# Kernel optimization log

Hardware: AMD Instinct MI355X
Metric: run time of the kernel (lower is better)

## Reference

```python
import jax, jax.numpy as jnp
import numpy as np

DIM = 1024
HEADS = 16
HEAD_DIM = DIM // HEADS
SCALE = HEAD_DIM ** -0.5


def apply_rope(x, theta=10000.0):
    # x: [b, h, n, d]
    n, d = x.shape[2], x.shape[3]
    seq = jnp.arange(n, dtype=jnp.float32)
    inv = 1.0 / (theta ** (jnp.arange(0, d, 2, dtype=jnp.float32) / d))  # [d/2]
    freqs = seq[:, None] * inv[None, :]  # [n, d/2]
    cos = jnp.cos(freqs)[None, None]  # [1,1,n,d/2]
    sin = jnp.sin(freqs)[None, None]
    x1, x2 = jnp.split(x, 2, axis=-1)
    return jnp.concatenate([x1 * cos - x2 * sin, x1 * sin + x2 * cos], axis=-1)


def setup_inputs() -> dict:
    key = jax.random.key(0)
    ks = jax.random.split(key, 7)
    s = DIM ** -0.5
    return {
        "x": jax.random.normal(ks[0], (2, 2048, DIM), dtype=jnp.float32),
        "Wqkv": jax.random.normal(ks[1], (3 * DIM, DIM), dtype=jnp.float32) * s,
        "bqkv": jax.random.normal(ks[2], (3 * DIM,), dtype=jnp.float32) * 0.02,
        "Wpre": jax.random.normal(ks[3], (HEADS, HEADS), dtype=jnp.float32) * HEADS ** -0.5,
        "Wpost": jax.random.normal(ks[4], (HEADS, HEADS), dtype=jnp.float32) * HEADS ** -0.5,
        "Wout": jax.random.normal(ks[5], (DIM, DIM), dtype=jnp.float32) * s,
        "bout": jax.random.normal(ks[6], (DIM,), dtype=jnp.float32) * 0.02,
    }


def reference(x, Wqkv, bqkv, Wpre, Wpost, Wout, bout):
    b, n, _ = x.shape
    qkv = x @ Wqkv.T + bqkv  # [b, n, 3*dim]
    q, k, v = jnp.split(qkv, 3, axis=-1)
    # [b, n, dim] -> [b, h, n, d]
    reshape = lambda t: t.reshape(b, n, HEADS, HEAD_DIM).transpose(0, 2, 1, 3)
    q, k, v = reshape(q), reshape(k), reshape(v)
    q = apply_rope(q)
    k = apply_rope(k)
    logits = jnp.einsum('bhid,bhjd->bhij', q, k) * SCALE
    # pre-softmax talking heads: Linear(heads->heads), y[...,g] = sum_h x[...,h] * Wpre[g,h]
    logits = jnp.einsum('bhij,gh->bgij', logits, Wpre)
    attn = jax.nn.softmax(logits, axis=-1)
    attn = jnp.einsum('bhij,gh->bgij', attn, Wpost)
    out = jnp.einsum('bhij,bhjd->bhid', attn, v)
    out = out.transpose(0, 2, 1, 3).reshape(b, n, DIM)
    return out @ Wout.T + bout
```

## Files before the change

### kernel.cpp

```cpp
#include <hip/hip_runtime.h>
#include <cstddef>
#include <cstdint>

#define SEQ    2048
#define DMODEL 1024
#define NHEAD  16
#define HDIM   64
#define SCALE  0.125f
#define LOG2E  1.4426950408889634f

typedef _Float16 f16;
typedef unsigned short u16;
typedef unsigned int   u32;
typedef __attribute__((ext_vector_type(8))) _Float16 h8v;
typedef __attribute__((ext_vector_type(4))) _Float16 h4v;
typedef __attribute__((ext_vector_type(4))) float    f4v;

__device__ __forceinline__ u32 pkh(float a, float b) {
    u16 x = __builtin_bit_cast(u16, (f16)a);
    u16 y = __builtin_bit_cast(u16, (f16)b);
    return (u32)x | ((u32)y << 16);
}

__device__ __forceinline__ float fexp2(float x) {
#if __has_builtin(__builtin_amdgcn_exp2f)
    return __builtin_amdgcn_exp2f(x);
#else
    return exp2f(x);
#endif
}

__device__ __forceinline__ f4v mfma32(h8v a, h8v b, f4v c) {
    return __builtin_amdgcn_mfma_f32_16x16x32_f16(a, b, c, 0, 0, 0);
}
__device__ __forceinline__ f4v mfma16(h4v a, h4v b, f4v c) {
    return __builtin_amdgcn_mfma_f32_16x16x16f16(a, b, c, 0, 0, 0);
}

__global__ __launch_bounds__(256)
void cvt_f16_kernel(const float* __restrict__ x, const float* __restrict__ Wqkv,
                    const float* __restrict__ Wout,
                    f16* __restrict__ Xh, f16* __restrict__ Wqh, f16* __restrict__ Woh)
{
    size_t i = ((size_t)blockIdx.x * 256 + threadIdx.x) * 8;
    const float* src; f16* dst; size_t off;
    if (i < 4194304)      { src = x;    dst = Xh;  off = i; }
    else if (i < 7340032) { src = Wqkv; dst = Wqh; off = i - 4194304; }
    else                  { src = Wout; dst = Woh; off = i - 7340032; }
    float4 a = *(const float4*)&src[off];
    float4 b = *(const float4*)&src[off + 4];
    uint4 o;
    o.x = pkh(a.x, a.y); o.y = pkh(a.z, a.w);
    o.z = pkh(b.x, b.y); o.w = pkh(b.z, b.w);
    *(uint4*)&dst[off] = o;
}

__global__ __launch_bounds__(256)
void gemm_f16_kernel(const f16* __restrict__ A, const f16* __restrict__ B,
                     const float* __restrict__ bias, void* __restrict__ Cout,
                     int N, int K, int mode)
{
    __shared__ __align__(16) char Asb[8192];
    __shared__ __align__(16) char Bsb[8192];
    int tid = threadIdx.x;
    int w = tid >> 6, l = tid & 63, lr = l & 15, lc = l >> 4;
    int row0 = blockIdx.y * 128, col0 = blockIdx.x * 128;
    int wr = (w >> 1) * 64, wc = (w & 1) * 64;

    f4v acc[4][4];
    #pragma unroll
    for (int m = 0; m < 4; ++m)
        #pragma unroll
        for (int n = 0; n < 4; ++n) acc[m][n] = (f4v){0.f, 0.f, 0.f, 0.f};

    int r0 = tid >> 2, k0s = tid & 3;
    int r1 = (tid + 256) >> 2, k1s = tid & 3;

    uint4 ra0, ra1, rb0, rb1;
    ra0 = *(const uint4*)&A[(size_t)(row0 + r0) * K + k0s * 8];
    ra1 = *(const uint4*)&A[(size_t)(row0 + r1) * K + k1s * 8];
    rb0 = *(const uint4*)&B[(size_t)(col0 + r0) * K + k0s * 8];
    rb1 = *(const uint4*)&B[(size_t)(col0 + r1) * K + k1s * 8];

    int NT = K >> 5;
    for (int kt = 0; kt < NT; ++kt) {
        *(uint4*)(Asb + r0 * 64 + ((k0s ^ (r0 & 3)) << 4)) = ra0;
        *(uint4*)(Asb + r1 * 64 + ((k1s ^ (r1 & 3)) << 4)) = ra1;
        *(uint4*)(Bsb + r0 * 64 + ((k0s ^ (r0 & 3)) << 4)) = rb0;
        *(uint4*)(Bsb + r1 * 64 + ((k1s ^ (r1 & 3)) << 4)) = rb1;
        if (kt + 1 < NT) {
            int kk = (kt + 1) * 32;
            ra0 = *(const uint4*)&A[(size_t)(row0 + r0) * K + kk + k0s * 8];
            ra1 = *(const uint4*)&A[(size_t)(row0 + r1) * K + kk + k1s * 8];
            rb0 = *(const uint4*)&B[(size_t)(col0 + r0) * K + kk + k0s * 8];
            rb1 = *(const uint4*)&B[(size_t)(col0 + r1) * K + kk + k1s * 8];
        }
        __syncthreads();
        h8v af[4], bf[4];
        #pragma unroll
        for (int m = 0; m < 4; ++m) {
            int row = wr + m * 16 + lr;
            af[m] = *(h8v*)(Asb + row * 64 + ((lc ^ (row & 3)) << 4));
        }
        #pragma unroll
        for (int n = 0; n < 4; ++n) {
            int col = wc + n * 16 + lr;
            bf[n] = *(h8v*)(Bsb + col * 64 + ((lc ^ (col & 3)) << 4));
        }
        #pragma unroll
        for (int m = 0; m < 4; ++m)
            #pragma unroll
            for (int n = 0; n < 4; ++n)
                acc[m][n] = mfma32(af[m], bf[n], acc[m][n]);
        __syncthreads();
    }

    #pragma unroll
    for (int m = 0; m < 4; ++m)
        #pragma unroll
        for (int r = 0; r < 4; ++r) {
            int row = row0 + wr + m * 16 + lc * 4 + r;
            #pragma unroll
            for (int n = 0; n < 4; ++n) {
                int col = col0 + wc + n * 16 + lr;
                float v = acc[m][n][r] + bias[col];
                if (mode == 0) ((f16*)Cout)[(size_t)row * N + col] = (f16)v;
                else           ((float*)Cout)[(size_t)row * N + col] = v;
            }
        }
}

__global__ __launch_bounds__(256)
void pack_qk_kernel(const f16* __restrict__ QKVh, f16* __restrict__ Qh, f16* __restrict__ Kh)
{
    int gid = blockIdx.x * 256 + threadIdx.x;
    int i     = gid & 15;
    int t8    = (gid >> 4) & 3;
    int h     = (gid >> 6) & 15;
    int rh    = (gid >> 10) & 255;
    int which = (gid >> 18) & 1;
    int row = rh * 16 + i;
    int pos = row & (SEQ - 1);
    int b   = row >> 11;
    f16* dst = which ? Kh : Qh;

    h8v x1 = *(const h8v*)&QKVh[(size_t)row * 3072 + which * 1024 + h * 64 + t8 * 8];
    h8v x2 = *(const h8v*)&QKVh[(size_t)row * 3072 + which * 1024 + h * 64 + t8 * 8 + 32];

    float y1[8], y2[8];
    #pragma unroll
    for (int e = 0; e < 8; ++e) {
        int t = t8 * 8 + e;
        float inv = exp2f((float)(-2 * t) * (0.015625f * 13.287712379549449f));
        float ang = (float)pos * inv;
        float c, s;
        sincosf(ang, &s, &c);
        float a1 = (float)x1[e], a2 = (float)x2[e];
        y1[e] = a1 * c - a2 * s;
        y2[e] = a1 * s + a2 * c;
    }
    int it = pos >> 4;
    size_t b0 = (((((size_t)(b*128 + it)*16 + h)*2 + 0)*4 + t8)*16 + i)*8;
    size_t b1 = (((((size_t)(b*128 + it)*16 + h)*2 + 1)*4 + t8)*16 + i)*8;
    uint4 o0, o1;
    o0.x = pkh(y1[0], y1[1]); o0.y = pkh(y1[2], y1[3]);
    o0.z = pkh(y1[4], y1[5]); o0.w = pkh(y1[6], y1[7]);
    o1.x = pkh(y2[0], y2[1]); o1.y = pkh(y2[2], y2[3]);
    o1.z = pkh(y2[4], y2[5]); o1.w = pkh(y2[6], y2[7]);
    *(uint4*)(dst + b0) = o0;
    *(uint4*)(dst + b1) = o1;
}

__global__ __launch_bounds__(256)
void pack_v_kernel(const f16* __restrict__ QKVh, f16* __restrict__ Vt)
{
    int gid = blockIdx.x * 256 + threadIdx.x;
    int dd = gid & 15;
    int jc = (gid >> 4) & 3;
    int dt = (gid >> 6) & 3;
    int g  = (gid >> 8) & 15;
    int jt = (gid >> 12) & 63;
    int b  = (gid >> 18) & 1;
    int d = g * 64 + dt * 16 + dd;
    f16 v[8];
    #pragma unroll
    for (int e = 0; e < 8; ++e) {
        int j = jt * 32 + jc * 8 + e;
        v[e] = QKVh[(size_t)(b * SEQ + j) * 3072 + 2048 + d];
    }
    size_t off = ((((((size_t)b*64 + jt)*16 + g)*4 + dt)*4 + jc)*16 + dd)*8;
    uint4 o;
    o.x = pkh((float)v[0], (float)v[1]); o.y = pkh((float)v[2], (float)v[3]);
    o.z = pkh((float)v[4], (float)v[5]); o.w = pkh((float)v[6], (float)v[7]);
    *(uint4*)(Vt + off) = o;
}

__global__ __launch_bounds__(256)
void pack_ctx_kernel(const f16* __restrict__ Cp, f16* __restrict__ Ch)
{
    size_t i = ((size_t)blockIdx.x * 256 + threadIdx.x) * 8;
    h8v p0 = *(const h8v*)&Cp[i];
    h8v p1 = *(const h8v*)&Cp[i + 4194304];
    h8v p2 = *(const h8v*)&Cp[i + 8388608];
    h8v p3 = *(const h8v*)&Cp[i + 12582912];
    float s[8];
    #pragma unroll
    for (int e = 0; e < 8; ++e)
        s[e] = (float)p0[e] + (float)p1[e] + (float)p2[e] + (float)p3[e];
    uint4 o;
    o.x = pkh(s[0], s[1]); o.y = pkh(s[2], s[3]);
    o.z = pkh(s[4], s[5]); o.w = pkh(s[6], s[7]);
    *(uint4*)&Ch[i] = o;
}

template<int FULL>
__global__ __launch_bounds__(1024, 1)
void attn_core(const f16* __restrict__ Qh, const f16* __restrict__ Kh,
               const f16* __restrict__ Vt, const float* __restrict__ Wpre,
               const float* __restrict__ Wpost, const float* __restrict__ Zp,
               float* __restrict__ Zout, f16* __restrict__ Octx)
{
    __shared__ __align__(16) char ss[32768];
    __shared__ __align__(16) char es[FULL ? 32768 : 16];
    __shared__ float zred[FULL ? 512 : 8192];

    int tid = threadIdx.x;
    int wv = tid >> 6;
    int l  = tid & 63;
    int lr = l & 15;
    int lc = l >> 4;

    int bid   = blockIdx.x;
    int it2   = bid & 63;
    int b     = (bid >> 6) & 1;
    int split = bid >> 7;

    h4v wpre4;
    #pragma unroll
    for (int e = 0; e < 4; ++e) wpre4[e] = (f16)(Wpre[lr * 16 + lc * 4 + e] * (SCALE * LOG2E));
    h4v wpost;
    if (FULL) {
        #pragma unroll
        for (int e = 0; e < 4; ++e) wpost[e] = (f16)Wpost[lr * 16 + lc * 4 + e];
    }

    h8v qf[2][2];
    #pragma unroll
    for (int itl = 0; itl < 2; ++itl)
        #pragma unroll
        for (int ks = 0; ks < 2; ++ks) {
            size_t off = ((((size_t)((b*128 + it2*2 + itl)*16 + wv)*2 + ks)*4 + lc)*16 + lr)*8;
            qf[itl][ks] = *(const h8v*)(Qh + off);
        }

    if (FULL && tid < 512) {
        int itl = tid >> 8, g = (tid >> 4) & 15, i = tid & 15;
        size_t idx = (size_t)(b * 16 + g) * SEQ + it2 * 32 + itl * 16 + i;
        zred[tid] = log2f(Zp[idx] + Zp[65536 + idx] + Zp[131072 + idx] + Zp[196608 + idx]);
    }
    __syncthreads();

    float m4[2][4];
    if (FULL) {
        #pragma unroll
        for (int itl = 0; itl < 2; ++itl)
            #pragma unroll
            for (int r = 0; r < 4; ++r)
                m4[itl][r] = zred[itl * 256 + (lc * 4 + r) * 16 + lr];
    }

    f4v pv[2][4];
    if (FULL) {
        #pragma unroll
        for (int itl = 0; itl < 2; ++itl)
            #pragma unroll
            for (int dt = 0; dt < 4; ++dt) pv[itl][dt] = (f4v){0.f, 0.f, 0.f, 0.f};
    }
    float zacc[2][4] = {};

    int j0beg = split * 512;
    int jtbeg = j0beg >> 4;

    for (int s = 0; s < 16; ++s) {
        h8v kf[2][2];
        #pragma unroll
        for (int js = 0; js < 2; ++js)
            #pragma unroll
            for (int ks = 0; ks < 2; ++ks) {
                size_t off = ((((size_t)((b*128 + jtbeg + s*2 + js)*16 + wv)*2 + ks)*4 + lc)*16 + lr)*8;
                kf[js][ks] = *(const h8v*)(Kh + off);
            }
        h8v vf[4];
        if (FULL) {
            int jt32 = (j0beg >> 5) + s;
            #pragma unroll
            for (int dt = 0; dt < 4; ++dt) {
                size_t voff = (((((size_t)(b*64 + jt32)*16 + wv)*4 + dt)*4 + lc)*16 + lr)*8;
                vf[dt] = *(const h8v*)(Vt + voff);
            }
        }

        #pragma unroll
        for (int itl = 0; itl < 2; ++itl)
            #pragma unroll
            for (int js = 0; js < 2; ++js) {
                f4v q = (f4v){0.f, 0.f, 0.f, 0.f};
                q = mfma32(qf[itl][0], kf[js][0], q);
                q = mfma32(qf[itl][1], kf[js][1], q);
                #pragma unroll
                for (int r = 0; r < 4; ++r) {
                    int i = lc * 4 + r;
                    int addr = itl * 16384 + ((wv >> 2) * 2 + js) * 2048
                             + i * 128 + ((lr ^ i) << 3) + (wv & 3) * 2;
                    *(u16*)(ss + addr) = __builtin_bit_cast(u16, (f16)q[r]);
                }
            }
        __syncthreads();

        #pragma unroll
        for (int itl = 0; itl < 2; ++itl) {
            u32 a2p[4];
            #pragma unroll
            for (int tt = 0; tt < 2; ++tt) {
                int t = wv * 2 + tt;
                int addr = itl * 16384 + (lc * 2 + (t >> 4)) * 2048
                         + lr * 128 + (((t & 15) ^ lr) << 3);
                union { uint2 u; h4v v; } cv;
                cv.u = *(uint2*)(ss + addr);
                f4v s1 = mfma16(wpre4, cv.v, (f4v){0.f, 0.f, 0.f, 0.f});
                if (!FULL) {
                    #pragma unroll
                    for (int r = 0; r < 4; ++r) zacc[itl][r] += fexp2(s1[r]);
                } else {
                    h4v pf;
                    #pragma unroll
                    for (int r = 0; r < 4; ++r) pf[r] = (f16)fexp2(s1[r] - m4[itl][r]);
                    f4v a2 = mfma16(wpost, pf, (f4v){0.f, 0.f, 0.f, 0.f});
                    #pragma unroll
                    for (int r = 0; r < 4; ++r) {
                        u32 v = (u32)__builtin_bit_cast(u16, (f16)a2[r]);
                        if (tt) a2p[r] |= v << 16;
                        else    a2p[r]  = v;
                    }
                }
            }
            if (FULL) {
                #pragma unroll
                for (int r = 0; r < 4; ++r) {
                    int gq = lc * 4 + r;
                    int off = itl * 16384 + ((gq * 1024 + lr * 64 + wv * 4) ^ ((lr & 7) << 4));
                    *(u32*)(es + off) = a2p[r];
                }
            }
        }
        __syncthreads();

        if (FULL) {
            #pragma unroll
            for (int itl = 0; itl < 2; ++itl) {
                h8v af = *(h8v*)(es + itl * 16384
                                 + ((wv * 1024 + lr * 64 + lc * 16) ^ ((lr & 7) << 4)));
                #pragma unroll
                for (int dt = 0; dt < 4; ++dt)
                    pv[itl][dt] = mfma32(af, vf[dt], pv[itl][dt]);
            }
        }
    }

    if (!FULL) {
        #pragma unroll
        for (int itl = 0; itl < 2; ++itl)
            #pragma unroll
            for (int r = 0; r < 4; ++r)
                zred[itl * 4096 + ((lc * 4 + r) * 16 + lr) * 16 + wv] = zacc[itl][r];
        __syncthreads();
        if (tid < 512) {
            int itl = tid >> 8, gi = tid & 255;
            float z = 0.f;
            #pragma unroll
            for (int w2 = 0; w2 < 16; ++w2) z += zred[itl * 4096 + gi * 16 + w2];
            int g = gi >> 4, i = gi & 15;
            Zout[(size_t)split * 65536 + (size_t)(b * 16 + g) * SEQ + it2 * 32 + itl * 16 + i] = z;
        }
    } else {
        f16* dst = Octx + (size_t)split * 4194304;
        #pragma unroll
        for (int itl = 0; itl < 2; ++itl)
            #pragma unroll
            for (int dt = 0; dt < 4; ++dt)
                #pragma unroll
                for (int r = 0; r < 4; ++r) {
                    int row = it2 * 32 + itl * 16 + lc * 4 + r;
                    int col = wv * 64 + dt * 16 + lr;
                    dst[(size_t)(b * SEQ + row) * DMODEL + col] = (f16)pv[itl][dt][r];
                }
    }
}

extern "C" void kernel_launch(void* const* d_in, const int* in_sizes, int n_in,
                              void* d_out, int out_size, void* d_ws, size_t ws_size,
                              hipStream_t stream)
{
    const float* x     = (const float*)d_in[0];
    const float* Wqkv  = (const float*)d_in[1];
    const float* bqkv  = (const float*)d_in[2];
    const float* Wpre  = (const float*)d_in[3];
    const float* Wpost = (const float*)d_in[4];
    const float* Wout  = (const float*)d_in[5];
    const float* bout  = (const float*)d_in[6];
    float* out = (float*)d_out;

    float* ws = (float*)d_ws;
    f16*   QKVh = (f16*)(ws);
    f16*   CTXp = (f16*)(ws);
    f16*   Xh   = (f16*)(ws + 8388608);
    f16*   Wqh  = (f16*)(ws + 10485760);
    f16*   Woh  = (f16*)(ws + 12058624);
    f16*   Qh   = (f16*)(ws + 12582912);
    f16*   Kh   = (f16*)(ws + 14680064);
    f16*   Vt   = (f16*)(ws + 16777216);
    f16*   Ch   = (f16*)(ws + 18874368);
    float* Zp   = ws + 19922944;

    dim3 blk(256);
    cvt_f16_kernel<<<4096, blk, 0, stream>>>(x, Wqkv, Wout, Xh, Wqh, Woh);
    gemm_f16_kernel<<<dim3(24, 32), blk, 0, stream>>>(Xh, Wqh, bqkv, (void*)QKVh, 3072, 1024, 0);
    pack_qk_kernel<<<2048, blk, 0, stream>>>(QKVh, Qh, Kh);
    pack_v_kernel<<<2048, blk, 0, stream>>>(QKVh, Vt);
    attn_core<0><<<512, dim3(1024), 0, stream>>>(Qh, Kh, Vt, Wpre, Wpost, nullptr, Zp, nullptr);
    attn_core<1><<<512, dim3(1024), 0, stream>>>(Qh, Kh, Vt, Wpre, Wpost, Zp, nullptr, CTXp);
    pack_ctx_kernel<<<2048, blk, 0, stream>>>(CTXp, Ch);
    gemm_f16_kernel<<<dim3(8, 32), blk, 0, stream>>>(Ch, Woh, bout, (void*)out, 1024, 1024, 1);
}
```

Before: 220.9 us.

## Fuse f16 conversion and split reduction into GEMM loads; double attention key tile

```diff
diff --git a/kernel.cpp b/kernel.cpp
--- a/kernel.cpp
+++ b/kernel.cpp
@@ -37,28 +37,24 @@
     return __builtin_amdgcn_mfma_f32_16x16x16f16(a, b, c, 0, 0, 0);
 }
 
+__device__ __forceinline__ uint4 cvt8(const float* __restrict__ p) {
+    float4 a = *(const float4*)p;
+    float4 b = *(const float4*)(p + 4);
+    return make_uint4(pkh(a.x, a.y), pkh(a.z, a.w), pkh(b.x, b.y), pkh(b.z, b.w));
+}
+
+__device__ __forceinline__ uint4 sum4(const f16* __restrict__ p) {
+    h8v s = *(const h8v*)p;
+    s = s + *(const h8v*)(p + 4194304);
+    s = s + *(const h8v*)(p + 8388608);
+    s = s + *(const h8v*)(p + 12582912);
+    union { h8v v; uint4 u; } c; c.v = s;
+    return c.u;
+}
+
 __global__ __launch_bounds__(256)
-void cvt_f16_kernel(const float* __restrict__ x, const float* __restrict__ Wqkv,
-                    const float* __restrict__ Wout,
-                    f16* __restrict__ Xh, f16* __restrict__ Wqh, f16* __restrict__ Woh)
-{
-    size_t i = ((size_t)blockIdx.x * 256 + threadIdx.x) * 8;
-    const float* src; f16* dst; size_t off;
-    if (i < 4194304)      { src = x;    dst = Xh;  off = i; }
-    else if (i < 7340032) { src = Wqkv; dst = Wqh; off = i - 4194304; }
-    else                  { src = Wout; dst = Woh; off = i - 7340032; }
-    float4 a = *(const float4*)&src[off];
-    float4 b = *(const float4*)&src[off + 4];
-    uint4 o;
-    o.x = pkh(a.x, a.y); o.y = pkh(a.z, a.w);
-    o.z = pkh(b.x, b.y); o.w = pkh(b.z, b.w);
-    *(uint4*)&dst[off] = o;
-}
-
-__global__ __launch_bounds__(256)
-void gemm_f16_kernel(const f16* __restrict__ A, const f16* __restrict__ B,
-                     const float* __restrict__ bias, void* __restrict__ Cout,
-                     int N, int K, int mode)
+void gemm_qkv_kernel(const float* __restrict__ A, const float* __restrict__ B,
+                     const float* __restrict__ bias, f16* __restrict__ C)
 {
     __shared__ __align__(16) char Asb[8192];
     __shared__ __align__(16) char Bsb[8192];
@@ -73,27 +69,25 @@
         #pragma unroll
         for (int n = 0; n < 4; ++n) acc[m][n] = (f4v){0.f, 0.f, 0.f, 0.f};
 
-    int r0 = tid >> 2, k0s = tid & 3;
-    int r1 = (tid + 256) >> 2, k1s = tid & 3;
-
-    uint4 ra0, ra1, rb0, rb1;
-    ra0 = *(const uint4*)&A[(size_t)(row0 + r0) * K + k0s * 8];
-    ra1 = *(const uint4*)&A[(size_t)(row0 + r1) * K + k1s * 8];
-    rb0 = *(const uint4*)&B[(size_t)(col0 + r0) * K + k0s * 8];
-    rb1 = *(const uint4*)&B[(size_t)(col0 + r1) * K + k1s * 8];
-
-    int NT = K >> 5;
-    for (int kt = 0; kt < NT; ++kt) {
-        *(uint4*)(Asb + r0 * 64 + ((k0s ^ (r0 & 3)) << 4)) = ra0;
-        *(uint4*)(Asb + r1 * 64 + ((k1s ^ (r1 & 3)) << 4)) = ra1;
-        *(uint4*)(Bsb + r0 * 64 + ((k0s ^ (r0 & 3)) << 4)) = rb0;
-        *(uint4*)(Bsb + r1 * 64 + ((k1s ^ (r1 & 3)) << 4)) = rb1;
-        if (kt + 1 < NT) {
+    int r0 = tid >> 2, ks = tid & 3;
+    int r1 = r0 + 64;
+
+    uint4 ra0 = cvt8(&A[(size_t)(row0 + r0) * 1024 + ks * 8]);
+    uint4 ra1 = cvt8(&A[(size_t)(row0 + r1) * 1024 + ks * 8]);
+    uint4 rb0 = cvt8(&B[(size_t)(col0 + r0) * 1024 + ks * 8]);
+    uint4 rb1 = cvt8(&B[(size_t)(col0 + r1) * 1024 + ks * 8]);
+
+    for (int kt = 0; kt < 32; ++kt) {
+        *(uint4*)(Asb + r0 * 64 + ((ks ^ (r0 & 3)) << 4)) = ra0;
+        *(uint4*)(Asb + r1 * 64 + ((ks ^ (r1 & 3)) << 4)) = ra1;
+        *(uint4*)(Bsb + r0 * 64 + ((ks ^ (r0 & 3)) << 4)) = rb0;
+        *(uint4*)(Bsb + r1 * 64 + ((ks ^ (r1 & 3)) << 4)) = rb1;
+        if (kt + 1 < 32) {
             int kk = (kt + 1) * 32;
-            ra0 = *(const uint4*)&A[(size_t)(row0 + r0) * K + kk + k0s * 8];
-            ra1 = *(const uint4*)&A[(size_t)(row0 + r1) * K + kk + k1s * 8];
-            rb0 = *(const uint4*)&B[(size_t)(col0 + r0) * K + kk + k0s * 8];
-            rb1 = *(const uint4*)&B[(size_t)(col0 + r1) * K + kk + k1s * 8];
+            ra0 = cvt8(&A[(size_t)(row0 + r0) * 1024 + kk + ks * 8]);
+            ra1 = cvt8(&A[(size_t)(row0 + r1) * 1024 + kk + ks * 8]);
+            rb0 = cvt8(&B[(size_t)(col0 + r0) * 1024 + kk + ks * 8]);
+            rb1 = cvt8(&B[(size_t)(col0 + r1) * 1024 + kk + ks * 8]);
         }
         __syncthreads();
         h8v af[4], bf[4];
@@ -123,9 +117,77 @@
             #pragma unroll
             for (int n = 0; n < 4; ++n) {
                 int col = col0 + wc + n * 16 + lr;
-                float v = acc[m][n][r] + bias[col];
-                if (mode == 0) ((f16*)Cout)[(size_t)row * N + col] = (f16)v;
-                else           ((float*)Cout)[(size_t)row * N + col] = v;
+                C[(size_t)row * 3072 + col] = (f16)(acc[m][n][r] + bias[col]);
+            }
+        }
+}
+
+__global__ __launch_bounds__(256)
+void gemm_out_kernel(const f16* __restrict__ P, const float* __restrict__ B,
+                     const float* __restrict__ bias, float* __restrict__ C)
+{
+    __shared__ __align__(16) char Asb[8192];
+    __shared__ __align__(16) char Bsb[8192];
+    int tid = threadIdx.x;
+    int w = tid >> 6, l = tid & 63, lr = l & 15, lc = l >> 4;
+    int row0 = blockIdx.y * 128, col0 = blockIdx.x * 128;
+    int wr = (w >> 1) * 64, wc = (w & 1) * 64;
+
+    f4v acc[4][4];
+    #pragma unroll
+    for (int m = 0; m < 4; ++m)
+        #pragma unroll
+        for (int n = 0; n < 4; ++n) acc[m][n] = (f4v){0.f, 0.f, 0.f, 0.f};
+
+    int r0 = tid >> 2, ks = tid & 3;
+    int r1 = r0 + 64;
+
+    uint4 ra0 = sum4(&P[(size_t)(row0 + r0) * 1024 + ks * 8]);
+    uint4 ra1 = sum4(&P[(size_t)(row0 + r1) * 1024 + ks * 8]);
+    uint4 rb0 = cvt8(&B[(size_t)(col0 + r0) * 1024 + ks * 8]);
+    uint4 rb1 = cvt8(&B[(size_t)(col0 + r1) * 1024 + ks * 8]);
+
+    for (int kt = 0; kt < 32; ++kt) {
+        *(uint4*)(Asb + r0 * 64 + ((ks ^ (r0 & 3)) << 4)) = ra0;
+        *(uint4*)(Asb + r1 * 64 + ((ks ^ (r1 & 3)) << 4)) = ra1;
+        *(uint4*)(Bsb + r0 * 64 + ((ks ^ (r0 & 3)) << 4)) = rb0;
+        *(uint4*)(Bsb + r1 * 64 + ((ks ^ (r1 & 3)) << 4)) = rb1;
+        if (kt + 1 < 32) {
+            int kk = (kt + 1) * 32;
+            ra0 = sum4(&P[(size_t)(row0 + r0) * 1024 + kk + ks * 8]);
+            ra1 = sum4(&P[(size_t)(row0 + r1) * 1024 + kk + ks * 8]);
+            rb0 = cvt8(&B[(size_t)(col0 + r0) * 1024 + kk + ks * 8]);
+            rb1 = cvt8(&B[(size_t)(col0 + r1) * 1024 + kk + ks * 8]);
+        }
+        __syncthreads();
+        h8v af[4], bf[4];
+        #pragma unroll
+        for (int m = 0; m < 4; ++m) {
+            int row = wr + m * 16 + lr;
+            af[m] = *(h8v*)(Asb + row * 64 + ((lc ^ (row & 3)) << 4));
+        }
+        #pragma unroll
+        for (int n = 0; n < 4; ++n) {
+            int col = wc + n * 16 + lr;
+            bf[n] = *(h8v*)(Bsb + col * 64 + ((lc ^ (col & 3)) << 4));
+        }
+        #pragma unroll
+        for (int m = 0; m < 4; ++m)
+            #pragma unroll
+            for (int n = 0; n < 4; ++n)
+                acc[m][n] = mfma32(af[m], bf[n], acc[m][n]);
+        __syncthreads();
+    }
+
+    #pragma unroll
+    for (int m = 0; m < 4; ++m)
+        #pragma unroll
+        for (int r = 0; r < 4; ++r) {
+            int row = row0 + wr + m * 16 + lc * 4 + r;
+            #pragma unroll
+            for (int n = 0; n < 4; ++n) {
+                int col = col0 + wc + n * 16 + lr;
+                C[(size_t)row * 1024 + col] = acc[m][n][r] + bias[col];
             }
         }
 }
@@ -195,24 +257,6 @@
     *(uint4*)(Vt + off) = o;
 }
 
-__global__ __launch_bounds__(256)
-void pack_ctx_kernel(const f16* __restrict__ Cp, f16* __restrict__ Ch)
-{
-    size_t i = ((size_t)blockIdx.x * 256 + threadIdx.x) * 8;
-    h8v p0 = *(const h8v*)&Cp[i];
-    h8v p1 = *(const h8v*)&Cp[i + 4194304];
-    h8v p2 = *(const h8v*)&Cp[i + 8388608];
-    h8v p3 = *(const h8v*)&Cp[i + 12582912];
-    float s[8];
-    #pragma unroll
-    for (int e = 0; e < 8; ++e)
-        s[e] = (float)p0[e] + (float)p1[e] + (float)p2[e] + (float)p3[e];
-    uint4 o;
-    o.x = pkh(s[0], s[1]); o.y = pkh(s[2], s[3]);
-    o.z = pkh(s[4], s[5]); o.w = pkh(s[6], s[7]);
-    *(uint4*)&Ch[i] = o;
-}
-
 template<int FULL>
 __global__ __launch_bounds__(1024, 1)
 void attn_core(const f16* __restrict__ Qh, const f16* __restrict__ Kh,
@@ -220,8 +264,8 @@
                const float* __restrict__ Wpost, const float* __restrict__ Zp,
                float* __restrict__ Zout, f16* __restrict__ Octx)
 {
-    __shared__ __align__(16) char ss[32768];
-    __shared__ __align__(16) char es[FULL ? 32768 : 16];
+    __shared__ __align__(16) char ss[65536];
+    __shared__ __align__(16) char es[FULL ? 65536 : 16];
     __shared__ float zred[FULL ? 512 : 8192];
 
     int tid = threadIdx.x;
@@ -280,50 +324,55 @@
 
     int j0beg = split * 512;
     int jtbeg = j0beg >> 4;
-
-    for (int s = 0; s < 16; ++s) {
-        h8v kf[2][2];
-        #pragma unroll
-        for (int js = 0; js < 2; ++js)
-            #pragma unroll
-            for (int ks = 0; ks < 2; ++ks) {
-                size_t off = ((((size_t)((b*128 + jtbeg + s*2 + js)*16 + wv)*2 + ks)*4 + lc)*16 + lr)*8;
-                kf[js][ks] = *(const h8v*)(Kh + off);
-            }
-        h8v vf[4];
+    int jvbeg = j0beg >> 5;
+
+    for (int s = 0; s < 8; ++s) {
+        h8v vf0[4];
         if (FULL) {
-            int jt32 = (j0beg >> 5) + s;
+            int jt32 = jvbeg + s * 2;
             #pragma unroll
             for (int dt = 0; dt < 4; ++dt) {
                 size_t voff = (((((size_t)(b*64 + jt32)*16 + wv)*4 + dt)*4 + lc)*16 + lr)*8;
-                vf[dt] = *(const h8v*)(Vt + voff);
-            }
-        }
-
-        #pragma unroll
-        for (int itl = 0; itl < 2; ++itl)
-            #pragma unroll
-            for (int js = 0; js < 2; ++js) {
-                f4v q = (f4v){0.f, 0.f, 0.f, 0.f};
-                q = mfma32(qf[itl][0], kf[js][0], q);
-                q = mfma32(qf[itl][1], kf[js][1], q);
-                #pragma unroll
-                for (int r = 0; r < 4; ++r) {
-                    int i = lc * 4 + r;
-                    int addr = itl * 16384 + ((wv >> 2) * 2 + js) * 2048
-                             + i * 128 + ((lr ^ i) << 3) + (wv & 3) * 2;
-                    *(u16*)(ss + addr) = __builtin_bit_cast(u16, (f16)q[r]);
+                vf0[dt] = *(const h8v*)(Vt + voff);
+            }
+        }
+        #pragma unroll
+        for (int jsp = 0; jsp < 2; ++jsp) {
+            h8v kf[2][2];
+            #pragma unroll
+            for (int js2 = 0; js2 < 2; ++js2)
+                #pragma unroll
+                for (int ks = 0; ks < 2; ++ks) {
+                    int jt = jtbeg + s * 4 + jsp * 2 + js2;
+                    size_t off = ((((size_t)((b*128 + jt)*16 + wv)*2 + ks)*4 + lc)*16 + lr)*8;
+                    kf[js2][ks] = *(const h8v*)(Kh + off);
                 }
-            }
+            #pragma unroll
+            for (int itl = 0; itl < 2; ++itl)
+                #pragma unroll
+                for (int js2 = 0; js2 < 2; ++js2) {
+                    f4v q = (f4v){0.f, 0.f, 0.f, 0.f};
+                    q = mfma32(qf[itl][0], kf[js2][0], q);
+                    q = mfma32(qf[itl][1], kf[js2][1], q);
+                    int js = jsp * 2 + js2;
+                    #pragma unroll
+                    for (int r = 0; r < 4; ++r) {
+                        int i = lc * 4 + r;
+                        int addr = itl * 32768 + ((wv >> 2) * 4 + js) * 2048
+                                 + i * 128 + ((lr ^ i) << 3) + (wv & 3) * 2;
+                        *(u16*)(ss + addr) = __builtin_bit_cast(u16, (f16)q[r]);
+                    }
+                }
+        }
         __syncthreads();
 
         #pragma unroll
         for (int itl = 0; itl < 2; ++itl) {
-            u32 a2p[4];
-            #pragma unroll
-            for (int tt = 0; tt < 2; ++tt) {
-                int t = wv * 2 + tt;
-                int addr = itl * 16384 + (lc * 2 + (t >> 4)) * 2048
+            u32 a2p[4][2];
+            #pragma unroll
+            for (int tt = 0; tt < 4; ++tt) {
+                int t = wv * 4 + tt;
+                int addr = itl * 32768 + (lc * 4 + (t >> 4)) * 2048
                          + lr * 128 + (((t & 15) ^ lr) << 3);
                 union { uint2 u; h4v v; } cv;
                 cv.u = *(uint2*)(ss + addr);
@@ -339,8 +388,8 @@
                     #pragma unroll
                     for (int r = 0; r < 4; ++r) {
                         u32 v = (u32)__builtin_bit_cast(u16, (f16)a2[r]);
-                        if (tt) a2p[r] |= v << 16;
-                        else    a2p[r]  = v;
+                        if (tt & 1) a2p[r][tt >> 1] |= v << 16;
+                        else        a2p[r][tt >> 1]  = v;
                     }
                 }
             }
@@ -348,21 +397,36 @@
                 #pragma unroll
                 for (int r = 0; r < 4; ++r) {
                     int gq = lc * 4 + r;
-                    int off = itl * 16384 + ((gq * 1024 + lr * 64 + wv * 4) ^ ((lr & 7) << 4));
-                    *(u32*)(es + off) = a2p[r];
+                    int off = itl * 32768 + gq * 2048 + lr * 128
+                            + ((wv * 8) ^ ((lr & 7) << 4));
+                    *(uint2*)(es + off) = make_uint2(a2p[r][0], a2p[r][1]);
                 }
             }
         }
-        __syncthreads();
-
+        h8v vf1[4];
         if (FULL) {
+            int jt32 = jvbeg + s * 2 + 1;
+            #pragma unroll
+            for (int dt = 0; dt < 4; ++dt) {
+                size_t voff = (((((size_t)(b*64 + jt32)*16 + wv)*4 + dt)*4 + lc)*16 + lr)*8;
+                vf1[dt] = *(const h8v*)(Vt + voff);
+            }
+        }
+        __syncthreads();
+
+        if (FULL) {
             #pragma unroll
             for (int itl = 0; itl < 2; ++itl) {
-                h8v af = *(h8v*)(es + itl * 16384
-                                 + ((wv * 1024 + lr * 64 + lc * 16) ^ ((lr & 7) << 4)));
+                h8v af0 = *(h8v*)(es + itl * 32768 + wv * 2048 + lr * 128
+                                  + ((0 * 64 + lc * 16) ^ ((lr & 7) << 4)));
+                h8v af1 = *(h8v*)(es + itl * 32768 + wv * 2048 + lr * 128
+                                  + ((1 * 64 + lc * 16) ^ ((lr & 7) << 4)));
                 #pragma unroll
                 for (int dt = 0; dt < 4; ++dt)
-                    pv[itl][dt] = mfma32(af, vf[dt], pv[itl][dt]);
+                    pv[itl][dt] = mfma32(af0, vf0[dt], pv[itl][dt]);
+                #pragma unroll
+                for (int dt = 0; dt < 4; ++dt)
+                    pv[itl][dt] = mfma32(af1, vf1[dt], pv[itl][dt]);
             }
         }
     }
@@ -413,22 +477,16 @@
     float* ws = (float*)d_ws;
     f16*   QKVh = (f16*)(ws);
     f16*   CTXp = (f16*)(ws);
-    f16*   Xh   = (f16*)(ws + 8388608);
-    f16*   Wqh  = (f16*)(ws + 10485760);
-    f16*   Woh  = (f16*)(ws + 12058624);
     f16*   Qh   = (f16*)(ws + 12582912);
     f16*   Kh   = (f16*)(ws + 14680064);
     f16*   Vt   = (f16*)(ws + 16777216);
-    f16*   Ch   = (f16*)(ws + 18874368);
     float* Zp   = ws + 19922944;
 
     dim3 blk(256);
-    cvt_f16_kernel<<<4096, blk, 0, stream>>>(x, Wqkv, Wout, Xh, Wqh, Woh);
-    gemm_f16_kernel<<<dim3(24, 32), blk, 0, stream>>>(Xh, Wqh, bqkv, (void*)QKVh, 3072, 1024, 0);
+    gemm_qkv_kernel<<<dim3(24, 32), blk, 0, stream>>>(x, Wqkv, bqkv, QKVh);
     pack_qk_kernel<<<2048, blk, 0, stream>>>(QKVh, Qh, Kh);
     pack_v_kernel<<<2048, blk, 0, stream>>>(QKVh, Vt);
     attn_core<0><<<512, dim3(1024), 0, stream>>>(Qh, Kh, Vt, Wpre, Wpost, nullptr, Zp, nullptr);
     attn_core<1><<<512, dim3(1024), 0, stream>>>(Qh, Kh, Vt, Wpre, Wpost, Zp, nullptr, CTXp);
-    pack_ctx_kernel<<<2048, blk, 0, stream>>>(CTXp, Ch);
-    gemm_f16_kernel<<<dim3(8, 32), blk, 0, stream>>>(Ch, Woh, bout, (void*)out, 1024, 1024, 1);
-}
+    gemm_out_kernel<<<dim3(8, 32), blk, 0, stream>>>(CTXp, Wout, bout, out);
+}
```

After: 245.9 us. 11.3% more time.

## Double key tile per attention iteration and allow two stats blocks per CU

Applied to the files above, without the earlier changes.

```diff
diff --git a/kernel.cpp b/kernel.cpp
--- a/kernel.cpp
+++ b/kernel.cpp
@@ -214,15 +214,14 @@
 }
 
 template<int FULL>
-__global__ __launch_bounds__(1024, 1)
+__global__ __launch_bounds__(1024, FULL ? 1 : 2)
 void attn_core(const f16* __restrict__ Qh, const f16* __restrict__ Kh,
                const f16* __restrict__ Vt, const float* __restrict__ Wpre,
                const float* __restrict__ Wpost, const float* __restrict__ Zp,
                float* __restrict__ Zout, f16* __restrict__ Octx)
 {
-    __shared__ __align__(16) char ss[32768];
-    __shared__ __align__(16) char es[FULL ? 32768 : 16];
-    __shared__ float zred[FULL ? 512 : 8192];
+    __shared__ __align__(16) char ss[65536];
+    __shared__ __align__(16) char es[FULL ? 65536 : 16];
 
     int tid = threadIdx.x;
     int wv = tid >> 6;
@@ -253,20 +252,21 @@
             qf[itl][ks] = *(const h8v*)(Qh + off);
         }
 
-    if (FULL && tid < 512) {
-        int itl = tid >> 8, g = (tid >> 4) & 15, i = tid & 15;
-        size_t idx = (size_t)(b * 16 + g) * SEQ + it2 * 32 + itl * 16 + i;
-        zred[tid] = log2f(Zp[idx] + Zp[65536 + idx] + Zp[131072 + idx] + Zp[196608 + idx]);
-    }
-    __syncthreads();
-
     float m4[2][4];
     if (FULL) {
+        float* zrd = (float*)ss;
+        if (tid < 512) {
+            int itl = tid >> 8, g = (tid >> 4) & 15, i = tid & 15;
+            size_t idx = (size_t)(b * 16 + g) * SEQ + it2 * 32 + itl * 16 + i;
+            zrd[tid] = log2f(Zp[idx] + Zp[65536 + idx] + Zp[131072 + idx] + Zp[196608 + idx]);
+        }
+        __syncthreads();
         #pragma unroll
         for (int itl = 0; itl < 2; ++itl)
             #pragma unroll
             for (int r = 0; r < 4; ++r)
-                m4[itl][r] = zred[itl * 256 + (lc * 4 + r) * 16 + lr];
+                m4[itl][r] = zrd[itl * 256 + (lc * 4 + r) * 16 + lr];
+        __syncthreads();
     }
 
     f4v pv[2][4];
@@ -280,50 +280,55 @@
 
     int j0beg = split * 512;
     int jtbeg = j0beg >> 4;
-
-    for (int s = 0; s < 16; ++s) {
-        h8v kf[2][2];
-        #pragma unroll
-        for (int js = 0; js < 2; ++js)
-            #pragma unroll
-            for (int ks = 0; ks < 2; ++ks) {
-                size_t off = ((((size_t)((b*128 + jtbeg + s*2 + js)*16 + wv)*2 + ks)*4 + lc)*16 + lr)*8;
-                kf[js][ks] = *(const h8v*)(Kh + off);
-            }
-        h8v vf[4];
+    int jvbeg = j0beg >> 5;
+
+    for (int s = 0; s < 8; ++s) {
+        h8v vf0[4];
         if (FULL) {
-            int jt32 = (j0beg >> 5) + s;
+            int jt32 = jvbeg + s * 2;
             #pragma unroll
             for (int dt = 0; dt < 4; ++dt) {
                 size_t voff = (((((size_t)(b*64 + jt32)*16 + wv)*4 + dt)*4 + lc)*16 + lr)*8;
-                vf[dt] = *(const h8v*)(Vt + voff);
-            }
-        }
-
-        #pragma unroll
-        for (int itl = 0; itl < 2; ++itl)
-            #pragma unroll
-            for (int js = 0; js < 2; ++js) {
-                f4v q = (f4v){0.f, 0.f, 0.f, 0.f};
-                q = mfma32(qf[itl][0], kf[js][0], q);
-                q = mfma32(qf[itl][1], kf[js][1], q);
-                #pragma unroll
-                for (int r = 0; r < 4; ++r) {
-                    int i = lc * 4 + r;
-                    int addr = itl * 16384 + ((wv >> 2) * 2 + js) * 2048
-                             + i * 128 + ((lr ^ i) << 3) + (wv & 3) * 2;
-                    *(u16*)(ss + addr) = __builtin_bit_cast(u16, (f16)q[r]);
+                vf0[dt] = *(const h8v*)(Vt + voff);
+            }
+        }
+        #pragma unroll
+        for (int jsp = 0; jsp < 2; ++jsp) {
+            h8v kf[2][2];
+            #pragma unroll
+            for (int js2 = 0; js2 < 2; ++js2)
+                #pragma unroll
+                for (int ks = 0; ks < 2; ++ks) {
+                    int jt = jtbeg + s * 4 + jsp * 2 + js2;
+                    size_t off = ((((size_t)((b*128 + jt)*16 + wv)*2 + ks)*4 + lc)*16 + lr)*8;
+                    kf[js2][ks] = *(const h8v*)(Kh + off);
                 }
-            }
+            #pragma unroll
+            for (int itl = 0; itl < 2; ++itl)
+                #pragma unroll
+                for (int js2 = 0; js2 < 2; ++js2) {
+                    f4v q = (f4v){0.f, 0.f, 0.f, 0.f};
+                    q = mfma32(qf[itl][0], kf[js2][0], q);
+                    q = mfma32(qf[itl][1], kf[js2][1], q);
+                    int js = jsp * 2 + js2;
+                    #pragma unroll
+                    for (int r = 0; r < 4; ++r) {
+                        int i = lc * 4 + r;
+                        int addr = itl * 32768 + ((wv >> 2) * 4 + js) * 2048
+                                 + i * 128 + ((lr ^ i) << 3) + (wv & 3) * 2;
+                        *(u16*)(ss + addr) = __builtin_bit_cast(u16, (f16)q[r]);
+                    }
+                }
+        }
         __syncthreads();
 
         #pragma unroll
         for (int itl = 0; itl < 2; ++itl) {
-            u32 a2p[4];
-            #pragma unroll
-            for (int tt = 0; tt < 2; ++tt) {
-                int t = wv * 2 + tt;
-                int addr = itl * 16384 + (lc * 2 + (t >> 4)) * 2048
+            u32 a2p[4][2];
+            #pragma unroll
+            for (int tt = 0; tt < 4; ++tt) {
+                int t = wv * 4 + tt;
+                int addr = itl * 32768 + (lc * 4 + (t >> 4)) * 2048
                          + lr * 128 + (((t & 15) ^ lr) << 3);
                 union { uint2 u; h4v v; } cv;
                 cv.u = *(uint2*)(ss + addr);
@@ -339,8 +344,8 @@
                     #pragma unroll
                     for (int r = 0; r < 4; ++r) {
                         u32 v = (u32)__builtin_bit_cast(u16, (f16)a2[r]);
-                        if (tt) a2p[r] |= v << 16;
-                        else    a2p[r]  = v;
+                        if (tt & 1) a2p[r][tt >> 1] |= v << 16;
+                        else        a2p[r][tt >> 1]  = v;
                     }
                 }
             }
@@ -348,37 +353,53 @@
                 #pragma unroll
                 for (int r = 0; r < 4; ++r) {
                     int gq = lc * 4 + r;
-                    int off = itl * 16384 + ((gq * 1024 + lr * 64 + wv * 4) ^ ((lr & 7) << 4));
-                    *(u32*)(es + off) = a2p[r];
+                    int off = itl * 32768 + gq * 2048 + lr * 128
+                            + ((wv * 8) ^ ((lr & 7) << 4));
+                    *(uint2*)(es + off) = make_uint2(a2p[r][0], a2p[r][1]);
                 }
             }
         }
-        __syncthreads();
-
+        h8v vf1[4];
         if (FULL) {
+            int jt32 = jvbeg + s * 2 + 1;
+            #pragma unroll
+            for (int dt = 0; dt < 4; ++dt) {
+                size_t voff = (((((size_t)(b*64 + jt32)*16 + wv)*4 + dt)*4 + lc)*16 + lr)*8;
+                vf1[dt] = *(const h8v*)(Vt + voff);
+            }
+        }
+        __syncthreads();
+
+        if (FULL) {
             #pragma unroll
             for (int itl = 0; itl < 2; ++itl) {
-                h8v af = *(h8v*)(es + itl * 16384
-                                 + ((wv * 1024 + lr * 64 + lc * 16) ^ ((lr & 7) << 4)));
+                h8v af0 = *(h8v*)(es + itl * 32768 + wv * 2048 + lr * 128
+                                  + ((0 * 64 + lc * 16) ^ ((lr & 7) << 4)));
+                h8v af1 = *(h8v*)(es + itl * 32768 + wv * 2048 + lr * 128
+                                  + ((1 * 64 + lc * 16) ^ ((lr & 7) << 4)));
                 #pragma unroll
                 for (int dt = 0; dt < 4; ++dt)
-                    pv[itl][dt] = mfma32(af, vf[dt], pv[itl][dt]);
+                    pv[itl][dt] = mfma32(af0, vf0[dt], pv[itl][dt]);
+                #pragma unroll
+                for (int dt = 0; dt < 4; ++dt)
+                    pv[itl][dt] = mfma32(af1, vf1[dt], pv[itl][dt]);
             }
         }
     }
 
     if (!FULL) {
+        float* zrd = (float*)ss;
         #pragma unroll
         for (int itl = 0; itl < 2; ++itl)
             #pragma unroll
             for (int r = 0; r < 4; ++r)
-                zred[itl * 4096 + ((lc * 4 + r) * 16 + lr) * 16 + wv] = zacc[itl][r];
+                zrd[itl * 4096 + ((lc * 4 + r) * 16 + lr) * 16 + wv] = zacc[itl][r];
         __syncthreads();
         if (tid < 512) {
             int itl = tid >> 8, gi = tid & 255;
             float z = 0.f;
             #pragma unroll
-            for (int w2 = 0; w2 < 16; ++w2) z += zred[itl * 4096 + gi * 16 + w2];
+            for (int w2 = 0; w2 < 16; ++w2) z += zrd[itl * 4096 + gi * 16 + w2];
             int g = gi >> 4, i = gi & 15;
             Zout[(size_t)split * 65536 + (size_t)(b * 16 + g) * SEQ + it2 * 32 + itl * 16 + i] = z;
         }
```

Result: faster. 209.9 us (-5.0%).
